# Kernel tuning notes

Measured on AMD Instinct MI355X. Metric: run time of the kernel, lower is better.

Reference implementation:

```python
import jax, jax.numpy as jnp
import numpy as np

N_NODES = 50000
N_EDGES = 800000


def _gcn_conv(x, W, b, src, dst, deg_inv_sqrt, n_nodes):
    # PyG GCNConv: h = x @ W, then symmetric-normalized sum aggregation
    h = x @ W  # [N, F_out]
    norm = deg_inv_sqrt[src] * deg_inv_sqrt[dst]  # [E_aug]
    msg = h[src] * norm[:, None]  # [E_aug, F_out]
    out = jax.ops.segment_sum(msg, dst, num_segments=n_nodes)
    return out + b


def setup_inputs() -> dict:
    key = jax.random.key(0)
    k1, k2, k3, k4 = jax.random.split(key, 4)
    x = jax.random.normal(k1, (N_NODES, 128), dtype=jnp.float32)
    edge_index = jax.random.randint(k2, (2, N_EDGES), 0, N_NODES, dtype=jnp.int64)
    W1 = jax.random.normal(k3, (128, 64), dtype=jnp.float32) * (1.0 / np.sqrt(128))
    b1 = jnp.zeros((64,), dtype=jnp.float32)
    W2 = jax.random.normal(k4, (64, 32), dtype=jnp.float32) * (1.0 / np.sqrt(64))
    b2 = jnp.zeros((32,), dtype=jnp.float32)
    return {"x": x, "edge_index": edge_index, "W1": W1, "b1": b1, "W2": W2, "b2": b2}


def reference(x, edge_index, W1, b1, W2, b2):
    n_nodes = x.shape[0]
    # add self-loops (PyG GCNConv default)
    loop = jnp.arange(n_nodes, dtype=edge_index.dtype)
    src = jnp.concatenate([edge_index[0], loop])
    dst = jnp.concatenate([edge_index[1], loop])
    # symmetric normalization: deg from target index (gcn_norm)
    deg = jax.ops.segment_sum(jnp.ones_like(dst, dtype=x.dtype), dst, num_segments=n_nodes)
    deg_inv_sqrt = jnp.where(deg > 0, jax.lax.rsqrt(jnp.maximum(deg, 1.0)), 0.0)

    h = _gcn_conv(x, W1, b1, src, dst, deg_inv_sqrt, n_nodes)
    h = jax.nn.relu(h)
    # dropout is identity in eval mode (reference runs inference)
    out = _gcn_conv(h, W2, b2, src, dst, deg_inv_sqrt, n_nodes)
    return out
```

## Files before the change

### kernel.cpp

```cpp
#include <hip/hip_runtime.h>


#define F_IN 128
#define F_MID 64
#define F_OUT 32
#define NBLK 256

#define RFL(x) __builtin_amdgcn_readfirstlane(x)

__global__ __launch_bounds__(256) void k_hist(
    const int* __restrict__ dst, int E, int chunk, int nbuk,
    int* __restrict__ blockHist) {
    __shared__ int cnt[256];
    int t = threadIdx.x;
    cnt[t] = 0;
    __syncthreads();
    int e0 = blockIdx.x * chunk;
    int e1 = min(E, e0 + chunk);
    for (int e = e0 + t; e < e1; e += 256)
        atomicAdd(&cnt[dst[e] >> 8], 1);
    __syncthreads();
    if (t < nbuk) blockHist[blockIdx.x * nbuk + t] = cnt[t];
}

__global__ __launch_bounds__(NBLK) void k_scan_buckets(
    const int* __restrict__ blockHist, int nbuk,
    int* __restrict__ blockOff, int* __restrict__ bucketTotal) {
    __shared__ int s[NBLK];
    int b = blockIdx.x;
    int t = threadIdx.x;
    int v = blockHist[t * nbuk + b];
    s[t] = v;
    __syncthreads();
    for (int o = 1; o < NBLK; o <<= 1) {
        int add = (t >= o) ? s[t - o] : 0;
        __syncthreads();
        s[t] += add;
        __syncthreads();
    }
    blockOff[t * nbuk + b] = s[t] - v;
    if (t == NBLK - 1) bucketTotal[b] = s[t];
}

__global__ __launch_bounds__(256) void k_scan_starts(
    const int* __restrict__ bucketTotal, int nbuk, int E,
    int* __restrict__ bucketStart) {
    __shared__ int s[256];
    int t = threadIdx.x;
    int v = (t < nbuk) ? bucketTotal[t] : 0;
    s[t] = v;
    __syncthreads();
    for (int o = 1; o < 256; o <<= 1) {
        int add = (t >= o) ? s[t - o] : 0;
        __syncthreads();
        s[t] += add;
        __syncthreads();
    }
    if (t < nbuk) bucketStart[t] = s[t] - v;
    if (t == 0) bucketStart[nbuk] = E;
}

__global__ __launch_bounds__(256) void k_scatter_edges(
    const int* __restrict__ src, const int* __restrict__ dst, int E, int chunk,
    int nbuk, const int* __restrict__ blockOff, const int* __restrict__ bucketStart,
    int2* __restrict__ esort) {
    __shared__ int off[256];
    int t = threadIdx.x;
    if (t < nbuk) off[t] = blockOff[blockIdx.x * nbuk + t] + bucketStart[t];
    __syncthreads();
    int e0 = blockIdx.x * chunk;
    int e1 = min(E, e0 + chunk);
    for (int e = e0 + t; e < e1; e += 256) {
        int d = dst[e];
        int pos = atomicAdd(&off[d >> 8], 1);
        esort[pos] = make_int2(d, src[e]);
    }
}

__global__ __launch_bounds__(256) void k_bucket_csr(
    const int2* __restrict__ esort, const int* __restrict__ bucketStart, int n,
    int* __restrict__ rowstart, int* __restrict__ deg, float* __restrict__ dis,
    int* __restrict__ col) {
    __shared__ int cnt[256];
    __shared__ int s[256];
    __shared__ int cur[256];
    int b = blockIdx.x;
    int t = threadIdx.x;
    int node0 = b << 8;
    int e0 = bucketStart[b], e1 = bucketStart[b + 1];
    cnt[t] = 0;
    __syncthreads();
    for (int e = e0 + t; e < e1; e += 256)
        atomicAdd(&cnt[esort[e].x & 255], 1);
    __syncthreads();
    int v = cnt[t];
    s[t] = v;
    __syncthreads();
    for (int o = 1; o < 256; o <<= 1) {
        int add = (t >= o) ? s[t - o] : 0;
        __syncthreads();
        s[t] += add;
        __syncthreads();
    }
    int ex = s[t] - v;
    cur[t] = ex;
    int node = node0 + t;
    if (node < n) {
        rowstart[node] = e0 + ex;
        deg[node] = v;
        dis[node] = rsqrtf((float)(v + 1));
    }
    __syncthreads();
    for (int e = e0 + t; e < e1; e += 256) {
        int2 p = esort[e];
        int pos = atomicAdd(&cur[p.x & 255], 1);
        col[e0 + pos] = p.y;
    }
}

__global__ __launch_bounds__(256, 4) void k_gemm1(
    const float* __restrict__ x, const float* __restrict__ W1,
    const float* __restrict__ dis, float* __restrict__ g1, int n) {
    __shared__ float xs[64 * 129];
    int tid  = threadIdx.x;
    int row0 = blockIdx.x * 64;
    for (int i = tid; i < 64 * F_IN; i += 256) {
        int r = i >> 7, k = i & 127;
        int gr = row0 + r;
        xs[r * 129 + k] = (gr < n) ? x[(size_t)gr * F_IN + k] : 0.0f;
    }
    __syncthreads();
    int w = RFL(tid >> 6);
    int r = tid & 63;
    const float4* W4 = (const float4*)W1;
    float4 a0 = {0.f,0.f,0.f,0.f}, a1 = a0, a2 = a0, a3 = a0;
#pragma unroll 4
    for (int k = 0; k < F_IN; ++k) {
        float xv = xs[r * 129 + k];
        float4 w0 = W4[k * 16 + w * 4 + 0];
        float4 w1 = W4[k * 16 + w * 4 + 1];
        float4 w2 = W4[k * 16 + w * 4 + 2];
        float4 w3 = W4[k * 16 + w * 4 + 3];
        a0.x += xv * w0.x; a0.y += xv * w0.y; a0.z += xv * w0.z; a0.w += xv * w0.w;
        a1.x += xv * w1.x; a1.y += xv * w1.y; a1.z += xv * w1.z; a1.w += xv * w1.w;
        a2.x += xv * w2.x; a2.y += xv * w2.y; a2.z += xv * w2.z; a2.w += xv * w2.w;
        a3.x += xv * w3.x; a3.y += xv * w3.y; a3.z += xv * w3.z; a3.w += xv * w3.w;
    }
    int gr = row0 + r;
    if (gr < n) {
        float dv = dis[gr];
        a0.x *= dv; a0.y *= dv; a0.z *= dv; a0.w *= dv;
        a1.x *= dv; a1.y *= dv; a1.z *= dv; a1.w *= dv;
        a2.x *= dv; a2.y *= dv; a2.z *= dv; a2.w *= dv;
        a3.x *= dv; a3.y *= dv; a3.z *= dv; a3.w *= dv;
        float4* o4 = (float4*)&g1[(size_t)gr * F_MID + w * 16];
        o4[0] = a0; o4[1] = a1; o4[2] = a2; o4[3] = a3;
    }
}

__global__ __launch_bounds__(256) void k_gather1(
    const int* __restrict__ rowstart, const int* __restrict__ deg,
    const int* __restrict__ col, const float* __restrict__ g1,
    const float* __restrict__ dis, const float* __restrict__ b1,
    float* __restrict__ h, int n) {
    int wave = RFL(threadIdx.x >> 6);
    int f    = threadIdx.x & 63;
    int d    = blockIdx.x * 4 + wave;
    if (d >= n) return;
    int base = RFL(rowstart[d]);
    int cnt  = RFL(deg[d]);
    float a0 = g1[(size_t)d * F_MID + f];
    float a1 = 0.f, a2 = 0.f, a3 = 0.f, a4 = 0.f, a5 = 0.f, a6 = 0.f, a7 = 0.f;
    int j = 0;
    for (; j + 8 <= cnt; j += 8) {
        int s0 = col[base + j + 0], s1 = col[base + j + 1];
        int s2 = col[base + j + 2], s3 = col[base + j + 3];
        int s4 = col[base + j + 4], s5 = col[base + j + 5];
        int s6 = col[base + j + 6], s7 = col[base + j + 7];
        a0 += g1[(size_t)s0 * F_MID + f];
        a1 += g1[(size_t)s1 * F_MID + f];
        a2 += g1[(size_t)s2 * F_MID + f];
        a3 += g1[(size_t)s3 * F_MID + f];
        a4 += g1[(size_t)s4 * F_MID + f];
        a5 += g1[(size_t)s5 * F_MID + f];
        a6 += g1[(size_t)s6 * F_MID + f];
        a7 += g1[(size_t)s7 * F_MID + f];
    }
    for (; j + 4 <= cnt; j += 4) {
        int s0 = col[base + j + 0], s1 = col[base + j + 1];
        int s2 = col[base + j + 2], s3 = col[base + j + 3];
        a0 += g1[(size_t)s0 * F_MID + f];
        a1 += g1[(size_t)s1 * F_MID + f];
        a2 += g1[(size_t)s2 * F_MID + f];
        a3 += g1[(size_t)s3 * F_MID + f];
    }
    for (; j < cnt; ++j) a0 += g1[(size_t)col[base + j] * F_MID + f];
    float acc = ((a0 + a1) + (a2 + a3)) + ((a4 + a5) + (a6 + a7));
    h[(size_t)d * F_MID + f] = fmaxf(acc * dis[d] + b1[f], 0.0f);
}

__global__ __launch_bounds__(256, 4) void k_gemm2(
    const float* __restrict__ h, const float* __restrict__ W2,
    const float* __restrict__ dis, float* __restrict__ g2, int n) {
    __shared__ float hs[64 * 65];
    int tid  = threadIdx.x;
    int row0 = blockIdx.x * 64;
    for (int i = tid; i < 64 * F_MID; i += 256) {
        int r = i >> 6, k = i & 63;
        int gr = row0 + r;
        hs[r * 65 + k] = (gr < n) ? h[(size_t)gr * F_MID + k] : 0.0f;
    }
    __syncthreads();
    int w = RFL(tid >> 6);
    int r = tid & 63;
    const float4* W4 = (const float4*)W2;
    float4 a0 = {0.f,0.f,0.f,0.f}, a1 = a0;
#pragma unroll 4
    for (int k = 0; k < F_MID; ++k) {
        float hv = hs[r * 65 + k];
        float4 w0 = W4[k * 8 + w * 2 + 0];
        float4 w1 = W4[k * 8 + w * 2 + 1];
        a0.x += hv * w0.x; a0.y += hv * w0.y; a0.z += hv * w0.z; a0.w += hv * w0.w;
        a1.x += hv * w1.x; a1.y += hv * w1.y; a1.z += hv * w1.z; a1.w += hv * w1.w;
    }
    int gr = row0 + r;
    if (gr < n) {
        float dv = dis[gr];
        a0.x *= dv; a0.y *= dv; a0.z *= dv; a0.w *= dv;
        a1.x *= dv; a1.y *= dv; a1.z *= dv; a1.w *= dv;
        float4* o4 = (float4*)&g2[(size_t)gr * F_OUT + w * 8];
        o4[0] = a0; o4[1] = a1;
    }
}

__global__ __launch_bounds__(256) void k_gather2(
    const int* __restrict__ rowstart, const int* __restrict__ deg,
    const int* __restrict__ col, const float* __restrict__ g2,
    const float* __restrict__ dis, const float* __restrict__ b2,
    float* __restrict__ out, int n) {
    int wave = RFL(threadIdx.x >> 6);
    int lane = threadIdx.x & 63;
    int j    = lane & 31;
    int p    = lane >> 5;
    int d    = blockIdx.x * 4 + wave;
    if (d >= n) return;
    int base = RFL(rowstart[d]);
    int cnt  = RFL(deg[d]);
    float a0 = (p == 0) ? g2[(size_t)d * F_OUT + j] : 0.0f;
    float a1 = 0.f, a2 = 0.f, a3 = 0.f;
    int t = 0;
    for (; t + 8 <= cnt; t += 8) {
        int sA0 = col[base + t + 0], sA1 = col[base + t + 1];
        int sB0 = col[base + t + 2], sB1 = col[base + t + 3];
        int sC0 = col[base + t + 4], sC1 = col[base + t + 5];
        int sD0 = col[base + t + 6], sD1 = col[base + t + 7];
        int sA = p ? sA1 : sA0;
        int sB = p ? sB1 : sB0;
        int sC = p ? sC1 : sC0;
        int sD = p ? sD1 : sD0;
        a0 += g2[(size_t)sA * F_OUT + j];
        a1 += g2[(size_t)sB * F_OUT + j];
        a2 += g2[(size_t)sC * F_OUT + j];
        a3 += g2[(size_t)sD * F_OUT + j];
    }
    for (; t + 2 <= cnt; t += 2) {
        int s0 = col[base + t], s1 = col[base + t + 1];
        int s = p ? s1 : s0;
        a0 += g2[(size_t)s * F_OUT + j];
    }
    if (t < cnt) {
        int s = col[base + t];
        if (p == 0) a0 += g2[(size_t)s * F_OUT + j];
    }
    float acc = (a0 + a1) + (a2 + a3);
    acc += __shfl_xor(acc, 32);
    if (p == 0) out[(size_t)d * F_OUT + j] = acc * dis[d] + b2[j];
}

extern "C" void kernel_launch(void* const* d_in, const int* in_sizes, int n_in,
                              void* d_out, int out_size, void* d_ws, size_t ws_size,
                              hipStream_t stream) {
    const float* x  = (const float*)d_in[0];
    const int*   ei = (const int*)d_in[1];
    const float* W1 = (const float*)d_in[2];
    const float* b1 = (const float*)d_in[3];
    const float* W2 = (const float*)d_in[4];
    const float* b2 = (const float*)d_in[5];

    int n = in_sizes[0] / F_IN;
    int E = in_sizes[1] / 2;
    const int* src = ei;
    const int* dst = ei + E;

    int nbuk  = (n + 255) >> 8;
    int chunk = (E + NBLK - 1) / NBLK;

    char* ws = (char*)d_ws;
    size_t off = 0;
    auto alloc = [&](size_t bytes) {
        char* p = ws + off;
        off += (bytes + 255) & ~(size_t)255;
        return p;
    };
    int*   blockHist   = (int*)  alloc((size_t)NBLK * nbuk * 4);
    int*   blockOff    = (int*)  alloc((size_t)NBLK * nbuk * 4);
    int*   bucketTotal = (int*)  alloc((size_t)nbuk * 4);
    int*   bucketStart = (int*)  alloc((size_t)(nbuk + 1) * 4);
    int2*  esort       = (int2*) alloc((size_t)E * 8);
    int*   col         = (int*)  alloc((size_t)E * 4);
    int*   rowstart    = (int*)  alloc((size_t)n * 4);
    int*   deg         = (int*)  alloc((size_t)n * 4);
    float* dis         = (float*)alloc((size_t)n * 4);
    float* g1          = (float*)alloc((size_t)n * F_MID * 4);
    float* h           = (float*)alloc((size_t)n * F_MID * 4);
    float* g2          = (float*)alloc((size_t)n * F_OUT * 4);

    k_hist<<<NBLK, 256, 0, stream>>>(dst, E, chunk, nbuk, blockHist);
    k_scan_buckets<<<nbuk, NBLK, 0, stream>>>(blockHist, nbuk, blockOff, bucketTotal);
    k_scan_starts<<<1, 256, 0, stream>>>(bucketTotal, nbuk, E, bucketStart);
    k_scatter_edges<<<NBLK, 256, 0, stream>>>(src, dst, E, chunk, nbuk, blockOff,
                                              bucketStart, esort);
    k_bucket_csr<<<nbuk, 256, 0, stream>>>(esort, bucketStart, n, rowstart, deg, dis, col);

    k_gemm1<<<(n + 63) / 64, 256, 0, stream>>>(x, W1, dis, g1, n);
    k_gather1<<<(n + 3) / 4, 256, 0, stream>>>(rowstart, deg, col, g1, dis, b1, h, n);
    k_gemm2<<<(n + 63) / 64, 256, 0, stream>>>(h, W2, dis, g2, n);
    k_gather2<<<(n + 3) / 4, 256, 0, stream>>>(rowstart, deg, col, g2, dis, b2,
                                               (float*)d_out, n);
}
```

Before: 198.9 us.

## Pack sorted edges into single ints and vectorize gathers with float4 multi-edge lanes

Sorted edge records are packed into one 32-bit word (src shifted left by 8, low byte holding the destination's offset within its bucket), which halves the esort traffic during the scatter and CSR-build passes. Both gather kernels now have each lane load a float4 and split a wavefront into several slots that each handle a different neighbor. Partial sums are then combined with cross-lane shuffles. This cuts the number of memory instructions per row and keeps more independent neighbor loads in flight. The packing assumes node indices fit in 24 bits, and the shuffle reduction adds extra instructions.

```diff
diff --git a/kernel.cpp b/kernel.cpp
--- a/kernel.cpp
+++ b/kernel.cpp
@@ -7,6 +7,10 @@
 #define NBLK 256
 
 #define RFL(x) __builtin_amdgcn_readfirstlane(x)
+
+__device__ __forceinline__ void f4add(float4& a, const float4& b) {
+    a.x += b.x; a.y += b.y; a.z += b.z; a.w += b.w;
+}
 
 __global__ __launch_bounds__(256) void k_hist(
     const int* __restrict__ dst, int E, int chunk, int nbuk,
@@ -63,7 +67,7 @@
 __global__ __launch_bounds__(256) void k_scatter_edges(
     const int* __restrict__ src, const int* __restrict__ dst, int E, int chunk,
     int nbuk, const int* __restrict__ blockOff, const int* __restrict__ bucketStart,
-    int2* __restrict__ esort) {
+    int* __restrict__ esort) {
     __shared__ int off[256];
     int t = threadIdx.x;
     if (t < nbuk) off[t] = blockOff[blockIdx.x * nbuk + t] + bucketStart[t];
@@ -73,12 +77,12 @@
     for (int e = e0 + t; e < e1; e += 256) {
         int d = dst[e];
         int pos = atomicAdd(&off[d >> 8], 1);
-        esort[pos] = make_int2(d, src[e]);
+        esort[pos] = (src[e] << 8) | (d & 255);
     }
 }
 
 __global__ __launch_bounds__(256) void k_bucket_csr(
-    const int2* __restrict__ esort, const int* __restrict__ bucketStart, int n,
+    const int* __restrict__ esort, const int* __restrict__ bucketStart, int n,
     int* __restrict__ rowstart, int* __restrict__ deg, float* __restrict__ dis,
     int* __restrict__ col) {
     __shared__ int cnt[256];
@@ -91,7 +95,7 @@
     cnt[t] = 0;
     __syncthreads();
     for (int e = e0 + t; e < e1; e += 256)
-        atomicAdd(&cnt[esort[e].x & 255], 1);
+        atomicAdd(&cnt[esort[e] & 255], 1);
     __syncthreads();
     int v = cnt[t];
     s[t] = v;
@@ -112,9 +116,9 @@
     }
     __syncthreads();
     for (int e = e0 + t; e < e1; e += 256) {
-        int2 p = esort[e];
-        int pos = atomicAdd(&cur[p.x & 255], 1);
-        col[e0 + pos] = p.y;
+        int p = esort[e];
+        int pos = atomicAdd(&cur[p & 255], 1);
+        col[e0 + pos] = p >> 8;
     }
 }
 
@@ -164,39 +168,54 @@
     const float* __restrict__ dis, const float* __restrict__ b1,
     float* __restrict__ h, int n) {
     int wave = RFL(threadIdx.x >> 6);
-    int f    = threadIdx.x & 63;
+    int lane = threadIdx.x & 63;
+    int q    = lane & 15;
+    int slot = lane >> 4;
     int d    = blockIdx.x * 4 + wave;
     if (d >= n) return;
     int base = RFL(rowstart[d]);
     int cnt  = RFL(deg[d]);
-    float a0 = g1[(size_t)d * F_MID + f];
-    float a1 = 0.f, a2 = 0.f, a3 = 0.f, a4 = 0.f, a5 = 0.f, a6 = 0.f, a7 = 0.f;
+    const float4* G4 = (const float4*)g1;
+    float4 z = {0.f, 0.f, 0.f, 0.f};
+    float4 a0 = (slot == 0) ? G4[(size_t)d * 16 + q] : z;
+    float4 a1 = z, a2 = z, a3 = z;
     int j = 0;
-    for (; j + 8 <= cnt; j += 8) {
-        int s0 = col[base + j + 0], s1 = col[base + j + 1];
-        int s2 = col[base + j + 2], s3 = col[base + j + 3];
-        int s4 = col[base + j + 4], s5 = col[base + j + 5];
-        int s6 = col[base + j + 6], s7 = col[base + j + 7];
-        a0 += g1[(size_t)s0 * F_MID + f];
-        a1 += g1[(size_t)s1 * F_MID + f];
-        a2 += g1[(size_t)s2 * F_MID + f];
-        a3 += g1[(size_t)s3 * F_MID + f];
-        a4 += g1[(size_t)s4 * F_MID + f];
-        a5 += g1[(size_t)s5 * F_MID + f];
-        a6 += g1[(size_t)s6 * F_MID + f];
-        a7 += g1[(size_t)s7 * F_MID + f];
+    for (; j + 16 <= cnt; j += 16) {
+        int s0 = col[base + j + 0  + slot];
+        int s1 = col[base + j + 4  + slot];
+        int s2 = col[base + j + 8  + slot];
+        int s3 = col[base + j + 12 + slot];
+        float4 v0 = G4[(size_t)s0 * 16 + q];
+        float4 v1 = G4[(size_t)s1 * 16 + q];
+        float4 v2 = G4[(size_t)s2 * 16 + q];
+        float4 v3 = G4[(size_t)s3 * 16 + q];
+        f4add(a0, v0); f4add(a1, v1); f4add(a2, v2); f4add(a3, v3);
     }
     for (; j + 4 <= cnt; j += 4) {
-        int s0 = col[base + j + 0], s1 = col[base + j + 1];
-        int s2 = col[base + j + 2], s3 = col[base + j + 3];
-        a0 += g1[(size_t)s0 * F_MID + f];
-        a1 += g1[(size_t)s1 * F_MID + f];
-        a2 += g1[(size_t)s2 * F_MID + f];
-        a3 += g1[(size_t)s3 * F_MID + f];
-    }
-    for (; j < cnt; ++j) a0 += g1[(size_t)col[base + j] * F_MID + f];
-    float acc = ((a0 + a1) + (a2 + a3)) + ((a4 + a5) + (a6 + a7));
-    h[(size_t)d * F_MID + f] = fmaxf(acc * dis[d] + b1[f], 0.0f);
+        int s = col[base + j + slot];
+        float4 v = G4[(size_t)s * 16 + q];
+        f4add(a0, v);
+    }
+    if (slot < cnt - j) {
+        int s = col[base + j + slot];
+        float4 v = G4[(size_t)s * 16 + q];
+        f4add(a0, v);
+    }
+    f4add(a0, a1); f4add(a2, a3); f4add(a0, a2);
+    a0.x += __shfl_xor(a0.x, 16); a0.y += __shfl_xor(a0.y, 16);
+    a0.z += __shfl_xor(a0.z, 16); a0.w += __shfl_xor(a0.w, 16);
+    a0.x += __shfl_xor(a0.x, 32); a0.y += __shfl_xor(a0.y, 32);
+    a0.z += __shfl_xor(a0.z, 32); a0.w += __shfl_xor(a0.w, 32);
+    if (slot == 0) {
+        float dv = dis[d];
+        float4 bv = ((const float4*)b1)[q];
+        float4 o;
+        o.x = fmaxf(a0.x * dv + bv.x, 0.f);
+        o.y = fmaxf(a0.y * dv + bv.y, 0.f);
+        o.z = fmaxf(a0.z * dv + bv.z, 0.f);
+        o.w = fmaxf(a0.w * dv + bv.w, 0.f);
+        ((float4*)h)[(size_t)d * 16 + q] = o;
+    }
 }
 
 __global__ __launch_bounds__(256, 4) void k_gemm2(
@@ -240,41 +259,51 @@
     float* __restrict__ out, int n) {
     int wave = RFL(threadIdx.x >> 6);
     int lane = threadIdx.x & 63;
-    int j    = lane & 31;
-    int p    = lane >> 5;
+    int q    = lane & 7;
+    int slot = lane >> 3;
     int d    = blockIdx.x * 4 + wave;
     if (d >= n) return;
     int base = RFL(rowstart[d]);
     int cnt  = RFL(deg[d]);
-    float a0 = (p == 0) ? g2[(size_t)d * F_OUT + j] : 0.0f;
-    float a1 = 0.f, a2 = 0.f, a3 = 0.f;
-    int t = 0;
-    for (; t + 8 <= cnt; t += 8) {
-        int sA0 = col[base + t + 0], sA1 = col[base + t + 1];
-        int sB0 = col[base + t + 2], sB1 = col[base + t + 3];
-        int sC0 = col[base + t + 4], sC1 = col[base + t + 5];
-        int sD0 = col[base + t + 6], sD1 = col[base + t + 7];
-        int sA = p ? sA1 : sA0;
-        int sB = p ? sB1 : sB0;
-        int sC = p ? sC1 : sC0;
-        int sD = p ? sD1 : sD0;
-        a0 += g2[(size_t)sA * F_OUT + j];
-        a1 += g2[(size_t)sB * F_OUT + j];
-        a2 += g2[(size_t)sC * F_OUT + j];
-        a3 += g2[(size_t)sD * F_OUT + j];
-    }
-    for (; t + 2 <= cnt; t += 2) {
-        int s0 = col[base + t], s1 = col[base + t + 1];
-        int s = p ? s1 : s0;
-        a0 += g2[(size_t)s * F_OUT + j];
-    }
-    if (t < cnt) {
-        int s = col[base + t];
-        if (p == 0) a0 += g2[(size_t)s * F_OUT + j];
-    }
-    float acc = (a0 + a1) + (a2 + a3);
-    acc += __shfl_xor(acc, 32);
-    if (p == 0) out[(size_t)d * F_OUT + j] = acc * dis[d] + b2[j];
+    const float4* G4 = (const float4*)g2;
+    float4 z = {0.f, 0.f, 0.f, 0.f};
+    float4 a0 = (slot == 0) ? G4[(size_t)d * 8 + q] : z;
+    float4 a1 = z;
+    int j = 0;
+    for (; j + 16 <= cnt; j += 16) {
+        int s0 = col[base + j + slot];
+        int s1 = col[base + j + 8 + slot];
+        float4 v0 = G4[(size_t)s0 * 8 + q];
+        float4 v1 = G4[(size_t)s1 * 8 + q];
+        f4add(a0, v0); f4add(a1, v1);
+    }
+    for (; j + 8 <= cnt; j += 8) {
+        int s = col[base + j + slot];
+        float4 v = G4[(size_t)s * 8 + q];
+        f4add(a0, v);
+    }
+    if (slot < cnt - j) {
+        int s = col[base + j + slot];
+        float4 v = G4[(size_t)s * 8 + q];
+        f4add(a0, v);
+    }
+    f4add(a0, a1);
+    a0.x += __shfl_xor(a0.x, 8);  a0.y += __shfl_xor(a0.y, 8);
+    a0.z += __shfl_xor(a0.z, 8);  a0.w += __shfl_xor(a0.w, 8);
+    a0.x += __shfl_xor(a0.x, 16); a0.y += __shfl_xor(a0.y, 16);
+    a0.z += __shfl_xor(a0.z, 16); a0.w += __shfl_xor(a0.w, 16);
+    a0.x += __shfl_xor(a0.x, 32); a0.y += __shfl_xor(a0.y, 32);
+    a0.z += __shfl_xor(a0.z, 32); a0.w += __shfl_xor(a0.w, 32);
+    if (slot == 0) {
+        float dv = dis[d];
+        float4 bv = ((const float4*)b2)[q];
+        float4 o;
+        o.x = a0.x * dv + bv.x;
+        o.y = a0.y * dv + bv.y;
+        o.z = a0.z * dv + bv.z;
+        o.w = a0.w * dv + bv.w;
+        ((float4*)out)[(size_t)d * 8 + q] = o;
+    }
 }
 
 extern "C" void kernel_launch(void* const* d_in, const int* in_sizes, int n_in,
@@ -306,7 +335,7 @@
     int*   blockOff    = (int*)  alloc((size_t)NBLK * nbuk * 4);
     int*   bucketTotal = (int*)  alloc((size_t)nbuk * 4);
     int*   bucketStart = (int*)  alloc((size_t)(nbuk + 1) * 4);
-    int2*  esort       = (int2*) alloc((size_t)E * 8);
+    int*   esort       = (int*)  alloc((size_t)E * 4);
     int*   col         = (int*)  alloc((size_t)E * 4);
     int*   rowstart    = (int*)  alloc((size_t)n * 4);
     int*   deg         = (int*)  alloc((size_t)n * 4);
```

Measured after the change: 196.7 us. About the same (-1.1%).
